# Kernel tuning notes

Hardware: AMD Instinct MI355X
Metric: run time of the kernel (lower is better)

The kernel has to match this reference:

```python
import jax, jax.numpy as jnp
import numpy as np

N_HOST, N_FLOW, E = 20000, 200000, 600000
D_IN, D_H, D_OUT = 64, 128, 32
NEG_SLOPE = 0.01  # F.leaky_relu default


def setup_inputs() -> dict:
    key = jax.random.key(0)
    ks = jax.random.split(key, 20)

    def w(k, shape):
        # kaiming-uniform-ish init scale (matches Linear fan-in scaling)
        lim = 1.0 / np.sqrt(shape[0])
        return jax.random.uniform(k, shape, jnp.float32, -lim, lim)

    return {
        "x_host": jax.random.normal(ks[0], (N_HOST, D_IN), jnp.float32),
        "x_flow": jax.random.normal(ks[1], (N_FLOW, D_IN), jnp.float32),
        "src_hf": jax.random.randint(ks[2], (E,), 0, N_HOST, dtype=jnp.int32),
        "dst_hf": jax.random.randint(ks[3], (E,), 0, N_FLOW, dtype=jnp.int32),
        "src_fh": jax.random.randint(ks[4], (E,), 0, N_FLOW, dtype=jnp.int32),
        "dst_fh": jax.random.randint(ks[5], (E,), 0, N_HOST, dtype=jnp.int32),
        "W0_hf_l": w(ks[6], (D_IN, D_H)), "W0_hf_r": w(ks[7], (D_IN, D_H)),
        "b0_hf": jnp.zeros((D_H,), jnp.float32),
        "W0_fh_l": w(ks[8], (D_IN, D_H)), "W0_fh_r": w(ks[9], (D_IN, D_H)),
        "b0_fh": jnp.zeros((D_H,), jnp.float32),
        "W1_hf_l": w(ks[10], (D_H, D_H)), "W1_hf_r": w(ks[11], (D_H, D_H)),
        "b1_hf": jnp.zeros((D_H,), jnp.float32),
        "W1_fh_l": w(ks[12], (D_H, D_H)), "W1_fh_r": w(ks[13], (D_H, D_H)),
        "b1_fh": jnp.zeros((D_H,), jnp.float32),
        "W_out": w(ks[14], (D_H, D_OUT)),
        "b_out": jnp.zeros((D_OUT,), jnp.float32),
    }


def _seg_mean(x, src, dst, n_dst):
    """Mean-aggregate src-node features over edges into n_dst segments."""
    s = jax.ops.segment_sum(x[src], dst, num_segments=n_dst)      # [n_dst, d]
    cnt = jax.ops.segment_sum(jnp.ones(src.shape, x.dtype), dst, num_segments=n_dst)
    return s / jnp.clip(cnt, 1.0)[:, None]


def _sage(x_src, x_dst, src, dst, Wl, Wr, b, n_dst):
    # SAGEConv: lin_l(mean_agg) + bias + lin_r(x_dst)
    agg = _seg_mean(x_src, src, dst, n_dst)
    return agg @ Wl + b + x_dst @ Wr


def reference(x_host, x_flow, src_hf, dst_hf, src_fh, dst_fh,
              W0_hf_l, W0_hf_r, b0_hf, W0_fh_l, W0_fh_r, b0_fh,
              W1_hf_l, W1_hf_r, b1_hf, W1_fh_l, W1_fh_r, b1_fh,
              W_out, b_out):
    lrelu = lambda v: jnp.where(v > 0, v, NEG_SLOPE * v)

    # layer 0
    h_flow = lrelu(_sage(x_host, x_flow, src_hf, dst_hf, W0_hf_l, W0_hf_r, b0_hf, N_FLOW))
    h_host = lrelu(_sage(x_flow, x_host, src_fh, dst_fh, W0_fh_l, W0_fh_r, b0_fh, N_HOST))

    # layer 1
    g_flow = lrelu(_sage(h_host, h_flow, src_hf, dst_hf, W1_hf_l, W1_hf_r, b1_hf, N_FLOW))
    g_host = lrelu(_sage(h_flow, h_host, src_fh, dst_fh, W1_fh_l, W1_fh_r, b1_fh, N_HOST))
    del g_host  # computed (matches module) but only 'flow' feeds the head

    return g_flow @ W_out + b_out  # [N_FLOW, D_OUT]
```

## Files before the change

kernel.cpp:

```cpp
#include <hip/hip_runtime.h>


#define N_HOST 20000
#define N_FLOW 200000
#define NEDGE  600000
#define D_IN   64
#define D_H    128
#define D_OUT  32
#define NSEG   (N_FLOW + N_HOST)
#define NBKT_F 782
#define NBKT_H 313
#define NBKT   (NBKT_F + NBKT_H)
#define NBKT_PAD 1100
#define NEB    586

typedef unsigned short u16;
typedef unsigned int   u32;
typedef short bf16x8 __attribute__((ext_vector_type(8)));
typedef float f32x4  __attribute__((ext_vector_type(4)));
typedef float fx2    __attribute__((ext_vector_type(2)));
typedef unsigned int u32x4 __attribute__((ext_vector_type(4)));

__device__ __forceinline__ float bfh(u16 h) { return __uint_as_float(((u32)h) << 16); }
__device__ __forceinline__ u16 fbh(float f) {
    u32 u = __float_as_uint(f);
    return (u16)((u + 0x7fffu + ((u >> 16) & 1u)) >> 16);
}
__device__ __forceinline__ u32 packbf(float x, float y) {
    return (u32)fbh(x) | ((u32)fbh(y) << 16);
}
__device__ __forceinline__ void accp(fx2* a, uint4 u) {
    fx2 p;
    p.x = __uint_as_float(u.x << 16); p.y = __uint_as_float(u.x & 0xffff0000u); a[0] += p;
    p.x = __uint_as_float(u.y << 16); p.y = __uint_as_float(u.y & 0xffff0000u); a[1] += p;
    p.x = __uint_as_float(u.z << 16); p.y = __uint_as_float(u.z & 0xffff0000u); a[2] += p;
    p.x = __uint_as_float(u.w << 16); p.y = __uint_as_float(u.w & 0xffff0000u); a[3] += p;
}
__device__ __forceinline__ uint4 packp(const fx2* a, float inv) {
    uint4 o;
    o.x = packbf(a[0].x * inv, a[0].y * inv);
    o.y = packbf(a[1].x * inv, a[1].y * inv);
    o.z = packbf(a[2].x * inv, a[2].y * inv);
    o.w = packbf(a[3].x * inv, a[3].y * inv);
    return o;
}

template <int U>
__device__ __forceinline__ uint4 gmean(const u16* __restrict__ pool, int rs, int coff,
                                       const int* __restrict__ gcsr,
                                       const int* __restrict__ lcsr, int st0, bool fit,
                                       int st, int en) {
    fx2 a[4] = {};
    for (int e = st; e < en; e += U) {
        int n[U];
#pragma unroll
        for (int j = 0; j < U; j++)
            n[j] = (e + j < en) ? (fit ? lcsr[e + j - st0] : gcsr[e + j]) : -1;
        uint4 u[U];
#pragma unroll
        for (int j = 0; j < U; j++)
            u[j] = (n[j] >= 0) ? *(const uint4*)(pool + n[j] * rs + coff)
                               : make_uint4(0u, 0u, 0u, 0u);
#pragma unroll
        for (int j = 0; j < U; j++) accp(a, u[j]);
    }
    float inv = (en > st) ? 1.f / (float)(en - st) : 0.f;
    return packp(a, inv);
}

__global__ void k_pre(const float* __restrict__ W0_hf_l, const float* __restrict__ W0_hf_r,
                      const float* __restrict__ W0_fh_l, const float* __restrict__ W0_fh_r,
                      const float* __restrict__ W1_l, const float* __restrict__ W1_r,
                      const float* __restrict__ Wout,
                      u16* __restrict__ WT0_hf, u16* __restrict__ WT0_fh,
                      u16* __restrict__ WT1_l, u16* __restrict__ WT1_r,
                      u16* __restrict__ WTo,
                      const float* __restrict__ xf, const float* __restrict__ xh,
                      u16* __restrict__ xfb, u16* __restrict__ xhb,
                      const int* __restrict__ dst_hf, const int* __restrict__ dst_fh,
                      int* __restrict__ bcnt) {
    int b = blockIdx.x, t = threadIdx.x;
    if (b < 34) {
        u16 tmp[8];
        if (b < 32) {
            int e = (b & 7) * 2048 + t * 8;
            int n = e >> 7, k0 = e & 127;
            if (b < 8) {
#pragma unroll
                for (int j = 0; j < 8; j++) {
                    int k = k0 + j;
                    tmp[j] = fbh(k < 64 ? W0_hf_l[k * D_H + n] : W0_hf_r[(k - 64) * D_H + n]);
                }
                *(uint4*)(WT0_hf + n * 128 + k0) = *(uint4*)tmp;
            } else if (b < 16) {
#pragma unroll
                for (int j = 0; j < 8; j++) {
                    int k = k0 + j;
                    tmp[j] = fbh(k < 64 ? W0_fh_l[k * D_H + n] : W0_fh_r[(k - 64) * D_H + n]);
                }
                *(uint4*)(WT0_fh + n * 128 + k0) = *(uint4*)tmp;
            } else if (b < 24) {
#pragma unroll
                for (int j = 0; j < 8; j++) tmp[j] = fbh(W1_l[(k0 + j) * D_H + n]);
                *(uint4*)(WT1_l + n * 128 + k0) = *(uint4*)tmp;
            } else {
#pragma unroll
                for (int j = 0; j < 8; j++) tmp[j] = fbh(W1_r[(k0 + j) * D_H + n]);
                *(uint4*)(WT1_r + n * 128 + k0) = *(uint4*)tmp;
            }
        } else {
            int e = (b - 32) * 2048 + t * 8;
            int n = e >> 7, k0 = e & 127;
#pragma unroll
            for (int j = 0; j < 8; j++) tmp[j] = fbh(Wout[(k0 + j) * D_OUT + n]);
            *(uint4*)(WTo + n * 128 + k0) = *(uint4*)tmp;
        }
    } else if (b < 34 + 6875) {
        int q = (b - 34) * 256 + t;
        const int TF = (N_FLOW * D_IN) / 8;
        const int TT = TF + (N_HOST * D_IN) / 8;
        if (q >= TT) return;
        const float* src; u16* dst; int base;
        if (q < TF) { src = xf; dst = xfb; base = q * 8; }
        else        { src = xh; dst = xhb; base = (q - TF) * 8; }
        float4 f0 = *(const float4*)(src + base);
        float4 f1 = *(const float4*)(src + base + 4);
        uint4 o;
        o.x = packbf(f0.x, f0.y); o.y = packbf(f0.z, f0.w);
        o.z = packbf(f1.x, f1.y); o.w = packbf(f1.z, f1.w);
        *(uint4*)(dst + base) = o;
    } else {
        __shared__ int h[NBKT];
        for (int j = t; j < NBKT; j += 256) h[j] = 0;
        __syncthreads();
        int base = (b - 34 - 6875) * 2048;
#pragma unroll
        for (int i = 0; i < 8; i++) {
            int e = base + t + i * 256;
            if (e < 2 * NEDGE) {
                int bkt = (e < NEDGE) ? (dst_hf[e] >> 8)
                                      : (NBKT_F + (dst_fh[e - NEDGE] >> 6));
                atomicAdd(&h[bkt], 1);
            }
        }
        __syncthreads();
        for (int j = t; j < NBKT; j += 256)
            if (h[j]) atomicAdd(&bcnt[j], h[j]);
    }
}

__global__ __launch_bounds__(256) void kb2(
    const int* __restrict__ src_hf, const int* __restrict__ dst_hf,
    const int* __restrict__ src_fh, const int* __restrict__ dst_fh,
    const int* __restrict__ bcnt, int* __restrict__ bcur,
    int2* __restrict__ binE) {
    __shared__ int spx[NBKT_PAD];
    __shared__ int ts[256];
    __shared__ int lh[NBKT];
    __shared__ int lb[NBKT];
    int t = threadIdx.x;
    int v[5], loc[5];
    int b5 = t * 5, s = 0;
#pragma unroll
    for (int j = 0; j < 5; j++) {
        int idx = b5 + j;
        v[j] = (idx < NBKT) ? bcnt[idx] : 0;
        loc[j] = s; s += v[j];
    }
    ts[t] = s;
    for (int j = t; j < NBKT; j += 256) lh[j] = 0;
    __syncthreads();
    for (int d = 1; d < 256; d <<= 1) {
        int x = (t >= d) ? ts[t - d] : 0;
        __syncthreads();
        ts[t] += x;
        __syncthreads();
    }
    int ex = ts[t] - s;
#pragma unroll
    for (int j = 0; j < 5; j++) {
        int idx = b5 + j;
        if (idx < NBKT_PAD) spx[idx] = ex + loc[j];
    }
    __syncthreads();
    int base = blockIdx.x * 2048;
    int mybkt[8], myrank[8], mysrc[8], mydst[8];
#pragma unroll
    for (int i = 0; i < 8; i++) {
        int e = base + t + i * 256;
        mybkt[i] = -1;
        if (e < 2 * NEDGE) {
            int sv, d;
            if (e < NEDGE) { sv = src_hf[e]; d = dst_hf[e]; }
            else           { sv = src_fh[e - NEDGE]; d = dst_fh[e - NEDGE] + N_FLOW; }
            int bkt = (d < N_FLOW) ? (d >> 8) : (NBKT_F + ((d - N_FLOW) >> 6));
            mybkt[i] = bkt; mysrc[i] = sv; mydst[i] = d;
            myrank[i] = atomicAdd(&lh[bkt], 1);
        }
    }
    __syncthreads();
    for (int j = t; j < NBKT; j += 256)
        lb[j] = lh[j] ? atomicAdd(&bcur[j], lh[j]) : 0;
    __syncthreads();
#pragma unroll
    for (int i = 0; i < 8; i++) {
        if (mybkt[i] >= 0) {
            int pos = spx[mybkt[i]] + lb[mybkt[i]] + myrank[i];
            binE[pos] = make_int2(mysrc[i], mydst[i]);
        }
    }
}

__global__ __launch_bounds__(256) void kb3(const int2* __restrict__ binE,
                                           const int* __restrict__ bcnt,
                                           int* __restrict__ off, int* __restrict__ csr) {
    __shared__ int sinc[NBKT_PAD];
    __shared__ int ts[256];
    __shared__ int deg[256];
    int b = blockIdx.x, t = threadIdx.x;
    int v[5], iv[5];
    int b5 = t * 5, s = 0;
#pragma unroll
    for (int j = 0; j < 5; j++) {
        int idx = b5 + j;
        v[j] = (idx < NBKT) ? bcnt[idx] : 0;
        s += v[j]; iv[j] = s;
    }
    ts[t] = s;
    __syncthreads();
    for (int d = 1; d < 256; d <<= 1) {
        int x = (t >= d) ? ts[t - d] : 0;
        __syncthreads();
        ts[t] += x;
        __syncthreads();
    }
    int ex = ts[t] - s;
#pragma unroll
    for (int j = 0; j < 5; j++) {
        int idx = b5 + j;
        if (idx < NBKT_PAD) sinc[idx] = ex + iv[j];
    }
    deg[t] = 0;
    __syncthreads();
    int e0 = (b == 0) ? 0 : sinc[b - 1];
    int e1 = sinc[b];
    int nbase, ncnt;
    if (b < NBKT_F) { nbase = b << 8; ncnt = min(256, N_FLOW - nbase); }
    else { int hb = b - NBKT_F; nbase = N_FLOW + (hb << 6); ncnt = min(64, NSEG - nbase); }
    for (int e = e0 + t; e < e1; e += 256) {
        int2 p = binE[e];
        atomicAdd(&deg[p.y - nbase], 1);
    }
    __syncthreads();
    int myd = deg[t];
    ts[t] = myd;
    __syncthreads();
    for (int d = 1; d < 256; d <<= 1) {
        int x = (t >= d) ? ts[t - d] : 0;
        __syncthreads();
        ts[t] += x;
        __syncthreads();
    }
    int st_ = e0 + ts[t] - myd;
    __syncthreads();
    deg[t] = st_;
    if (t < ncnt) off[nbase + t] = st_ + myd;
    __syncthreads();
    for (int e = e0 + t; e < e1; e += 256) {
        int2 p = binE[e];
        int r = atomicAdd(&deg[p.y - nbase], 1);
        csr[r] = p.x;
    }
}

__global__ __launch_bounds__(512, 4) void k_host(
    const u16* __restrict__ xfb, const u16* __restrict__ xhb,
    const int* __restrict__ off, const int* __restrict__ csr,
    const u16* __restrict__ WT0, const float* __restrict__ b0,
    const u16* __restrict__ WT1l, u16* __restrict__ hT, int M) {
    __shared__ __align__(16) u16 sA[64 * 136];
    __shared__ int sOff[72];
    __shared__ int sCsr[2560];
    const int t = threadIdx.x;
    const int m0 = blockIdx.x * 64;
    if (t < 65) {
        int idx = N_FLOW + m0 - 1 + t;
        sOff[t] = off[min(idx, NSEG - 1)];
    }
    {
        int r = t >> 3, c = t & 7;
        int row = m0 + r;
        uint4 v = make_uint4(0u, 0u, 0u, 0u);
        if (row < M) v = *(const uint4*)(xhb + row * 64 + c * 8);
        *(uint4*)(&sA[r * 136 + 64 + c * 8]) = v;
    }
    __syncthreads();
    int st0 = sOff[0];
    int win = sOff[64] - st0;
    bool fit = (win <= 2560);
    if (fit) for (int e = t; e < win; e += 512) sCsr[e] = csr[st0 + e];
    __syncthreads();
    {
        int r = t >> 3, c = t & 7;
        int row = m0 + r;
        uint4 o = make_uint4(0u, 0u, 0u, 0u);
        if (row < M) o = gmean<8>(xfb, 64, c * 8, csr, sCsr, st0, fit, sOff[r], sOff[r + 1]);
        *(uint4*)(&sA[r * 136 + c * 8]) = o;
    }
    __syncthreads();
    const int w = t >> 6, wr = w >> 1, wc = w & 1;
    const int ln = t & 63, l15 = ln & 15, quad = ln >> 4;
    const u16* pA = sA + (wr * 16 + l15) * 136 + quad * 8;
    const u16* pB0 = WT0 + wc * 8192 + l15 * 128 + quad * 8;
    f32x4 acc[4];
#pragma unroll
    for (int tt = 0; tt < 4; tt++) acc[tt] = (f32x4){0.f, 0.f, 0.f, 0.f};
#pragma unroll
    for (int s = 0; s < 4; s++) {
        bf16x8 a = *(const bf16x8*)(pA + s * 32);
#pragma unroll
        for (int tt = 0; tt < 4; tt++) {
            bf16x8 b = *(const bf16x8*)(pB0 + tt * 2048 + s * 32);
            acc[tt] = __builtin_amdgcn_mfma_f32_16x16x32_bf16(a, b, acc[tt], 0, 0, 0);
        }
    }
    __syncthreads();
#pragma unroll
    for (int tt = 0; tt < 4; tt++) {
        int col = wc * 64 + tt * 16 + l15;
        float bv = b0[col];
#pragma unroll
        for (int i = 0; i < 4; i++) {
            int rl = wr * 16 + quad * 4 + i;
            float v = acc[tt][i] + bv;
            v = v > 0.f ? v : 0.01f * v;
            sA[rl * 136 + col] = fbh(v);
        }
    }
    __syncthreads();
    const u16* pB1 = WT1l + wc * 8192 + l15 * 128 + quad * 8;
    f32x4 accB[4];
#pragma unroll
    for (int tt = 0; tt < 4; tt++) accB[tt] = (f32x4){0.f, 0.f, 0.f, 0.f};
#pragma unroll
    for (int s = 0; s < 4; s++) {
        bf16x8 a = *(const bf16x8*)(pA + s * 32);
#pragma unroll
        for (int tt = 0; tt < 4; tt++) {
            bf16x8 b = *(const bf16x8*)(pB1 + tt * 2048 + s * 32);
            accB[tt] = __builtin_amdgcn_mfma_f32_16x16x32_bf16(a, b, accB[tt], 0, 0, 0);
        }
    }
#pragma unroll
    for (int tt = 0; tt < 4; tt++) {
        int col = wc * 64 + tt * 16 + l15;
#pragma unroll
        for (int i = 0; i < 4; i++) {
            int row = m0 + wr * 16 + quad * 4 + i;
            if (row < M) hT[row * D_H + col] = fbh(accB[tt][i]);
        }
    }
}

__global__ __launch_bounds__(512, 8) void k_mega(
    const u16* __restrict__ xfb, const u16* __restrict__ xhb,
    const int* __restrict__ off, const int* __restrict__ csr,
    const u16* __restrict__ hT,
    const u16* __restrict__ WT0, const float* __restrict__ b0,
    const u16* __restrict__ WT1r, const float* __restrict__ b1,
    const u16* __restrict__ WTo, const float* __restrict__ bout,
    float* __restrict__ OUT) {
    __shared__ __align__(16) u16 sA[64 * 136];
    __shared__ __align__(16) u16 sAg[64 * 136];
    __shared__ int sOff[72];
    __shared__ int sCsr[1024];
    const int t = threadIdx.x;
    const int m0 = blockIdx.x * 64;
    if (t < 65) {
        int idx = m0 - 1 + t;
        sOff[t] = (idx < 0) ? 0 : off[idx];
    }
    {
        int r = t >> 3, c = t & 7;
        const u32x4* p = (const u32x4*)(xfb + (m0 + r) * 64 + c * 8);
        u32x4 v = __builtin_nontemporal_load(p);
        *(u32x4*)(&sA[r * 136 + 64 + c * 8]) = v;
    }
    __syncthreads();
    int st0 = sOff[0];
    int win = sOff[64] - st0;
    bool fit = (win <= 1024);
    if (fit) for (int e = t; e < win; e += 512)
        sCsr[e] = __builtin_nontemporal_load(csr + st0 + e);
    __syncthreads();
    {
        int r = t >> 3, c = t & 7;
        uint4 o = gmean<4>(xhb, 64, c * 8, csr, sCsr, st0, fit, sOff[r], sOff[r + 1]);
        *(uint4*)(&sA[r * 136 + c * 8]) = o;
    }
#pragma unroll
    for (int i = 0; i < 2; i++) {
        int q = t + i * 512;
        int r = q >> 4, c = q & 15;
        uint4 o = gmean<4>(hT, 128, c * 8, csr, sCsr, st0, fit, sOff[r], sOff[r + 1]);
        *(uint4*)(&sAg[r * 136 + c * 8]) = o;
    }
    __syncthreads();
    const int w = t >> 6, wr = w >> 1, wc = w & 1;
    const int ln = t & 63, l15 = ln & 15, quad = ln >> 4;
    const u16* pA = sA + (wr * 16 + l15) * 136 + quad * 8;
    const u16* pB0 = WT0 + wc * 8192 + l15 * 128 + quad * 8;
    f32x4 acc[4];
#pragma unroll
    for (int tt = 0; tt < 4; tt++) acc[tt] = (f32x4){0.f, 0.f, 0.f, 0.f};
#pragma unroll
    for (int s = 0; s < 4; s++) {
        bf16x8 av = *(const bf16x8*)(pA + s * 32);
#pragma unroll
        for (int tt = 0; tt < 4; tt++) {
            bf16x8 b = *(const bf16x8*)(pB0 + tt * 2048 + s * 32);
            acc[tt] = __builtin_amdgcn_mfma_f32_16x16x32_bf16(av, b, acc[tt], 0, 0, 0);
        }
    }
    __syncthreads();
#pragma unroll
    for (int tt = 0; tt < 4; tt++) {
        int col = wc * 64 + tt * 16 + l15;
        float bv = b0[col];
#pragma unroll
        for (int i = 0; i < 4; i++) {
            int rl = wr * 16 + quad * 4 + i;
            float v = acc[tt][i] + bv;
            v = v > 0.f ? v : 0.01f * v;
            sA[rl * 136 + col] = fbh(v);
        }
    }
    __syncthreads();
    const u16* pB1 = WT1r + wc * 8192 + l15 * 128 + quad * 8;
    f32x4 accB[4];
#pragma unroll
    for (int tt = 0; tt < 4; tt++) accB[tt] = (f32x4){0.f, 0.f, 0.f, 0.f};
#pragma unroll
    for (int s = 0; s < 4; s++) {
        bf16x8 av = *(const bf16x8*)(pA + s * 32);
#pragma unroll
        for (int tt = 0; tt < 4; tt++) {
            bf16x8 b = *(const bf16x8*)(pB1 + tt * 2048 + s * 32);
            accB[tt] = __builtin_amdgcn_mfma_f32_16x16x32_bf16(av, b, accB[tt], 0, 0, 0);
        }
    }
#pragma unroll
    for (int tt = 0; tt < 4; tt++) {
        int col = wc * 64 + tt * 16 + l15;
        float bv = b1[col];
#pragma unroll
        for (int i = 0; i < 4; i++) {
            int rl = wr * 16 + quad * 4 + i;
            float v = accB[tt][i] + bfh(sAg[rl * 136 + col]) + bv;
            v = v > 0.f ? v : 0.01f * v;
            sAg[rl * 136 + col] = fbh(v);
        }
    }
    __syncthreads();
    const u16* pG = sAg + (wr * 16 + l15) * 136 + quad * 8;
    const u16* pBo = WTo + wc * 2048 + l15 * 128 + quad * 8;
    f32x4 acc2 = (f32x4){0.f, 0.f, 0.f, 0.f};
#pragma unroll
    for (int s = 0; s < 4; s++) {
        bf16x8 g = *(const bf16x8*)(pG + s * 32);
        bf16x8 b = *(const bf16x8*)(pBo + s * 32);
        acc2 = __builtin_amdgcn_mfma_f32_16x16x32_bf16(g, b, acc2, 0, 0, 0);
    }
    {
        int col = wc * 16 + l15;
        float bv = bout[col];
#pragma unroll
        for (int i = 0; i < 4; i++) {
            int row = m0 + wr * 16 + quad * 4 + i;
            __builtin_nontemporal_store(acc2[i] + bv, &OUT[row * D_OUT + col]);
        }
    }
}

extern "C" void kernel_launch(void* const* d_in, const int* in_sizes, int n_in,
                              void* d_out, int out_size, void* d_ws, size_t ws_size,
                              hipStream_t stream) {
    const float* x_host  = (const float*)d_in[0];
    const float* x_flow  = (const float*)d_in[1];
    const int* src_hf  = (const int*)d_in[2];
    const int* dst_hf  = (const int*)d_in[3];
    const int* src_fh  = (const int*)d_in[4];
    const int* dst_fh  = (const int*)d_in[5];
    const float* W0_hf_l = (const float*)d_in[6];
    const float* W0_hf_r = (const float*)d_in[7];
    const float* b0_hf   = (const float*)d_in[8];
    const float* W0_fh_l = (const float*)d_in[9];
    const float* W0_fh_r = (const float*)d_in[10];
    const float* b0_fh   = (const float*)d_in[11];
    const float* W1_hf_l = (const float*)d_in[12];
    const float* W1_hf_r = (const float*)d_in[13];
    const float* b1_hf   = (const float*)d_in[14];
    const float* W_out   = (const float*)d_in[18];
    const float* b_out   = (const float*)d_in[19];
    float* out = (float*)d_out;

    char* ws = (char*)d_ws;
    int*  off    = (int*)(ws + 0);
    int*  csr    = (int*)(ws + 880000);
    u16*  hT     = (u16*)(ws + 5680000);
    int*  bcnt   = (int*)(ws + 5680000);
    int*  bcur   = (int*)(ws + 5684380);
    u16*  xfb    = (u16*)(ws + 10800000);
    u16*  xhb    = (u16*)(ws + 36400000);
    int2* binE   = (int2*)(ws + 38960000);
    u16*  WT0_hf = (u16*)(ws + 48562560);
    u16*  WT0_fh = (u16*)(ws + 48595328);
    u16*  WT1_l  = (u16*)(ws + 48628096);
    u16*  WT1_r  = (u16*)(ws + 48660864);
    u16*  WTo    = (u16*)(ws + 48693632);

    (void)hipMemsetAsync(bcnt, 0, 8760, stream);
    k_pre<<<34 + 6875 + NEB, 256, 0, stream>>>(
        W0_hf_l, W0_hf_r, W0_fh_l, W0_fh_r, W1_hf_l, W1_hf_r, W_out,
        WT0_hf, WT0_fh, WT1_l, WT1_r, WTo,
        x_flow, x_host, xfb, xhb, dst_hf, dst_fh, bcnt);
    kb2<<<NEB, 256, 0, stream>>>(src_hf, dst_hf, src_fh, dst_fh, bcnt, bcur, binE);
    kb3<<<NBKT, 256, 0, stream>>>(binE, bcnt, off, csr);
    k_host<<<313, 512, 0, stream>>>(xfb, xhb, off, csr, WT0_fh, b0_fh, WT1_l, hT, N_HOST);
    k_mega<<<3125, 512, 0, stream>>>(xfb, xhb, off, csr, hT, WT0_hf, b0_hf,
                                     WT1_r, b1_hf, WTo, b_out, out);
}
```

Measured before the change: 337.5 us.

## Merge graph CSR build stages into one cooperative kernel with grid syncs

```diff
diff --git a/kernel.cpp b/kernel.cpp
--- a/kernel.cpp
+++ b/kernel.cpp
@@ -1,4 +1,6 @@
 #include <hip/hip_runtime.h>
+#include <hip/hip_cooperative_groups.h>
+namespace cg = cooperative_groups;
 
 
 #define N_HOST 20000
@@ -76,9 +78,7 @@
                       u16* __restrict__ WT1_l, u16* __restrict__ WT1_r,
                       u16* __restrict__ WTo,
                       const float* __restrict__ xf, const float* __restrict__ xh,
-                      u16* __restrict__ xfb, u16* __restrict__ xhb,
-                      const int* __restrict__ dst_hf, const int* __restrict__ dst_fh,
-                      int* __restrict__ bcnt) {
+                      u16* __restrict__ xfb, u16* __restrict__ xhb) {
     int b = blockIdx.x, t = threadIdx.x;
     if (b < 34) {
         u16 tmp[8];
@@ -115,7 +115,7 @@
             for (int j = 0; j < 8; j++) tmp[j] = fbh(Wout[(k0 + j) * D_OUT + n]);
             *(uint4*)(WTo + n * 128 + k0) = *(uint4*)tmp;
         }
-    } else if (b < 34 + 6875) {
+    } else {
         int q = (b - 34) * 256 + t;
         const int TF = (N_FLOW * D_IN) / 8;
         const int TT = TF + (N_HOST * D_IN) / 8;
@@ -129,147 +129,158 @@
         o.x = packbf(f0.x, f0.y); o.y = packbf(f0.z, f0.w);
         o.z = packbf(f1.x, f1.y); o.w = packbf(f1.z, f1.w);
         *(uint4*)(dst + base) = o;
-    } else {
-        __shared__ int h[NBKT];
-        for (int j = t; j < NBKT; j += 256) h[j] = 0;
-        __syncthreads();
-        int base = (b - 34 - 6875) * 2048;
+    }
+}
+
+__global__ __launch_bounds__(256) void k_graph(
+    const int* __restrict__ src_hf, const int* __restrict__ dst_hf,
+    const int* __restrict__ src_fh, const int* __restrict__ dst_fh,
+    int* __restrict__ bcnt, int* __restrict__ bcur,
+    int2* __restrict__ binE, int* __restrict__ off, int* __restrict__ csr) {
+    __shared__ int sh_h[NBKT];
+    __shared__ int sh_spx[NBKT_PAD];
+    __shared__ int sh_lb[NBKT];
+    __shared__ int sh_ts[256];
+    __shared__ int sh_deg[256];
+    cg::grid_group grid = cg::this_grid();
+    const int b = blockIdx.x, t = threadIdx.x;
+
+    {
+        int i = b * 256 + t;
+        if (i < NBKT) { bcnt[i] = 0; bcur[i] = 0; }
+    }
+    __threadfence();
+    grid.sync();
+
+    if (b < NEB) {
+        for (int j = t; j < NBKT; j += 256) sh_h[j] = 0;
+        __syncthreads();
+        int base = b * 2048;
 #pragma unroll
         for (int i = 0; i < 8; i++) {
             int e = base + t + i * 256;
             if (e < 2 * NEDGE) {
                 int bkt = (e < NEDGE) ? (dst_hf[e] >> 8)
                                       : (NBKT_F + (dst_fh[e - NEDGE] >> 6));
-                atomicAdd(&h[bkt], 1);
+                atomicAdd(&sh_h[bkt], 1);
             }
         }
         __syncthreads();
         for (int j = t; j < NBKT; j += 256)
-            if (h[j]) atomicAdd(&bcnt[j], h[j]);
-    }
-}
-
-__global__ __launch_bounds__(256) void kb2(
-    const int* __restrict__ src_hf, const int* __restrict__ dst_hf,
-    const int* __restrict__ src_fh, const int* __restrict__ dst_fh,
-    const int* __restrict__ bcnt, int* __restrict__ bcur,
-    int2* __restrict__ binE) {
-    __shared__ int spx[NBKT_PAD];
-    __shared__ int ts[256];
-    __shared__ int lh[NBKT];
-    __shared__ int lb[NBKT];
-    int t = threadIdx.x;
-    int v[5], loc[5];
-    int b5 = t * 5, s = 0;
-#pragma unroll
-    for (int j = 0; j < 5; j++) {
-        int idx = b5 + j;
-        v[j] = (idx < NBKT) ? bcnt[idx] : 0;
-        loc[j] = s; s += v[j];
-    }
-    ts[t] = s;
-    for (int j = t; j < NBKT; j += 256) lh[j] = 0;
-    __syncthreads();
-    for (int d = 1; d < 256; d <<= 1) {
-        int x = (t >= d) ? ts[t - d] : 0;
-        __syncthreads();
-        ts[t] += x;
-        __syncthreads();
-    }
-    int ex = ts[t] - s;
-#pragma unroll
-    for (int j = 0; j < 5; j++) {
-        int idx = b5 + j;
-        if (idx < NBKT_PAD) spx[idx] = ex + loc[j];
-    }
-    __syncthreads();
-    int base = blockIdx.x * 2048;
-    int mybkt[8], myrank[8], mysrc[8], mydst[8];
-#pragma unroll
-    for (int i = 0; i < 8; i++) {
-        int e = base + t + i * 256;
-        mybkt[i] = -1;
-        if (e < 2 * NEDGE) {
-            int sv, d;
-            if (e < NEDGE) { sv = src_hf[e]; d = dst_hf[e]; }
-            else           { sv = src_fh[e - NEDGE]; d = dst_fh[e - NEDGE] + N_FLOW; }
-            int bkt = (d < N_FLOW) ? (d >> 8) : (NBKT_F + ((d - N_FLOW) >> 6));
-            mybkt[i] = bkt; mysrc[i] = sv; mydst[i] = d;
-            myrank[i] = atomicAdd(&lh[bkt], 1);
-        }
-    }
-    __syncthreads();
-    for (int j = t; j < NBKT; j += 256)
-        lb[j] = lh[j] ? atomicAdd(&bcur[j], lh[j]) : 0;
-    __syncthreads();
-#pragma unroll
-    for (int i = 0; i < 8; i++) {
-        if (mybkt[i] >= 0) {
-            int pos = spx[mybkt[i]] + lb[mybkt[i]] + myrank[i];
-            binE[pos] = make_int2(mysrc[i], mydst[i]);
-        }
-    }
-}
-
-__global__ __launch_bounds__(256) void kb3(const int2* __restrict__ binE,
-                                           const int* __restrict__ bcnt,
-                                           int* __restrict__ off, int* __restrict__ csr) {
-    __shared__ int sinc[NBKT_PAD];
-    __shared__ int ts[256];
-    __shared__ int deg[256];
-    int b = blockIdx.x, t = threadIdx.x;
-    int v[5], iv[5];
-    int b5 = t * 5, s = 0;
-#pragma unroll
-    for (int j = 0; j < 5; j++) {
-        int idx = b5 + j;
-        v[j] = (idx < NBKT) ? bcnt[idx] : 0;
-        s += v[j]; iv[j] = s;
-    }
-    ts[t] = s;
-    __syncthreads();
-    for (int d = 1; d < 256; d <<= 1) {
-        int x = (t >= d) ? ts[t - d] : 0;
-        __syncthreads();
-        ts[t] += x;
-        __syncthreads();
-    }
-    int ex = ts[t] - s;
-#pragma unroll
-    for (int j = 0; j < 5; j++) {
-        int idx = b5 + j;
-        if (idx < NBKT_PAD) sinc[idx] = ex + iv[j];
-    }
-    deg[t] = 0;
-    __syncthreads();
-    int e0 = (b == 0) ? 0 : sinc[b - 1];
-    int e1 = sinc[b];
-    int nbase, ncnt;
-    if (b < NBKT_F) { nbase = b << 8; ncnt = min(256, N_FLOW - nbase); }
-    else { int hb = b - NBKT_F; nbase = N_FLOW + (hb << 6); ncnt = min(64, NSEG - nbase); }
-    for (int e = e0 + t; e < e1; e += 256) {
-        int2 p = binE[e];
-        atomicAdd(&deg[p.y - nbase], 1);
-    }
-    __syncthreads();
-    int myd = deg[t];
-    ts[t] = myd;
-    __syncthreads();
-    for (int d = 1; d < 256; d <<= 1) {
-        int x = (t >= d) ? ts[t - d] : 0;
-        __syncthreads();
-        ts[t] += x;
-        __syncthreads();
-    }
-    int st_ = e0 + ts[t] - myd;
-    __syncthreads();
-    deg[t] = st_;
-    if (t < ncnt) off[nbase + t] = st_ + myd;
-    __syncthreads();
-    for (int e = e0 + t; e < e1; e += 256) {
-        int2 p = binE[e];
-        int r = atomicAdd(&deg[p.y - nbase], 1);
-        csr[r] = p.x;
+            if (sh_h[j]) atomicAdd(&bcnt[j], sh_h[j]);
+    }
+    __threadfence();
+    grid.sync();
+
+    if (b < NEB) {
+        int v[5], loc[5];
+        int b5 = t * 5, s = 0;
+#pragma unroll
+        for (int j = 0; j < 5; j++) {
+            int idx = b5 + j;
+            v[j] = (idx < NBKT) ? bcnt[idx] : 0;
+            loc[j] = s; s += v[j];
+        }
+        sh_ts[t] = s;
+        for (int j = t; j < NBKT; j += 256) sh_h[j] = 0;
+        __syncthreads();
+        for (int d = 1; d < 256; d <<= 1) {
+            int x = (t >= d) ? sh_ts[t - d] : 0;
+            __syncthreads();
+            sh_ts[t] += x;
+            __syncthreads();
+        }
+        int ex = sh_ts[t] - s;
+#pragma unroll
+        for (int j = 0; j < 5; j++) {
+            int idx = b5 + j;
+            if (idx < NBKT_PAD) sh_spx[idx] = ex + loc[j];
+        }
+        __syncthreads();
+        int base = b * 2048;
+        int mybkt[8], myrank[8], mysrc[8], mydst[8];
+#pragma unroll
+        for (int i = 0; i < 8; i++) {
+            int e = base + t + i * 256;
+            mybkt[i] = -1;
+            if (e < 2 * NEDGE) {
+                int sv, d;
+                if (e < NEDGE) { sv = src_hf[e]; d = dst_hf[e]; }
+                else           { sv = src_fh[e - NEDGE]; d = dst_fh[e - NEDGE] + N_FLOW; }
+                int bkt = (d < N_FLOW) ? (d >> 8) : (NBKT_F + ((d - N_FLOW) >> 6));
+                mybkt[i] = bkt; mysrc[i] = sv; mydst[i] = d;
+                myrank[i] = atomicAdd(&sh_h[bkt], 1);
+            }
+        }
+        __syncthreads();
+        for (int j = t; j < NBKT; j += 256)
+            sh_lb[j] = sh_h[j] ? atomicAdd(&bcur[j], sh_h[j]) : 0;
+        __syncthreads();
+#pragma unroll
+        for (int i = 0; i < 8; i++) {
+            if (mybkt[i] >= 0) {
+                int pos = sh_spx[mybkt[i]] + sh_lb[mybkt[i]] + myrank[i];
+                binE[pos] = make_int2(mysrc[i], mydst[i]);
+            }
+        }
+    }
+    __threadfence();
+    grid.sync();
+
+    {
+        int v[5], iv[5];
+        int b5 = t * 5, s = 0;
+#pragma unroll
+        for (int j = 0; j < 5; j++) {
+            int idx = b5 + j;
+            v[j] = (idx < NBKT) ? bcnt[idx] : 0;
+            s += v[j]; iv[j] = s;
+        }
+        sh_ts[t] = s;
+        __syncthreads();
+        for (int d = 1; d < 256; d <<= 1) {
+            int x = (t >= d) ? sh_ts[t - d] : 0;
+            __syncthreads();
+            sh_ts[t] += x;
+            __syncthreads();
+        }
+        int ex = sh_ts[t] - s;
+#pragma unroll
+        for (int j = 0; j < 5; j++) {
+            int idx = b5 + j;
+            if (idx < NBKT_PAD) sh_spx[idx] = ex + iv[j];
+        }
+        sh_deg[t] = 0;
+        __syncthreads();
+        int e0 = (b == 0) ? 0 : sh_spx[b - 1];
+        int e1 = sh_spx[b];
+        int nbase, ncnt;
+        if (b < NBKT_F) { nbase = b << 8; ncnt = min(256, N_FLOW - nbase); }
+        else { int hb = b - NBKT_F; nbase = N_FLOW + (hb << 6); ncnt = min(64, NSEG - nbase); }
+        for (int e = e0 + t; e < e1; e += 256) {
+            int2 p = binE[e];
+            atomicAdd(&sh_deg[p.y - nbase], 1);
+        }
+        __syncthreads();
+        int myd = sh_deg[t];
+        sh_ts[t] = myd;
+        __syncthreads();
+        for (int d = 1; d < 256; d <<= 1) {
+            int x = (t >= d) ? sh_ts[t - d] : 0;
+            __syncthreads();
+            sh_ts[t] += x;
+            __syncthreads();
+        }
+        int st_ = e0 + sh_ts[t] - myd;
+        __syncthreads();
+        sh_deg[t] = st_;
+        if (t < ncnt) off[nbase + t] = st_ + myd;
+        __syncthreads();
+        for (int e = e0 + t; e < e1; e += 256) {
+            int2 p = binE[e];
+            int r = atomicAdd(&sh_deg[p.y - nbase], 1);
+            csr[r] = p.x;
+        }
     }
 }
 
@@ -519,13 +530,17 @@
     u16*  WT1_r  = (u16*)(ws + 48660864);
     u16*  WTo    = (u16*)(ws + 48693632);
 
-    (void)hipMemsetAsync(bcnt, 0, 8760, stream);
-    k_pre<<<34 + 6875 + NEB, 256, 0, stream>>>(
+    k_pre<<<34 + 6875, 256, 0, stream>>>(
         W0_hf_l, W0_hf_r, W0_fh_l, W0_fh_r, W1_hf_l, W1_hf_r, W_out,
         WT0_hf, WT0_fh, WT1_l, WT1_r, WTo,
-        x_flow, x_host, xfb, xhb, dst_hf, dst_fh, bcnt);
-    kb2<<<NEB, 256, 0, stream>>>(src_hf, dst_hf, src_fh, dst_fh, bcnt, bcur, binE);
-    kb3<<<NBKT, 256, 0, stream>>>(binE, bcnt, off, csr);
+        x_flow, x_host, xfb, xhb);
+    {
+        void* kargs[] = {(void*)&src_hf, (void*)&dst_hf, (void*)&src_fh, (void*)&dst_fh,
+                         (void*)&bcnt, (void*)&bcur, (void*)&binE, (void*)&off,
+                         (void*)&csr};
+        (void)hipLaunchCooperativeKernel((const void*)k_graph, dim3(NBKT), dim3(256),
+                                         kargs, 0, stream);
+    }
     k_host<<<313, 512, 0, stream>>>(xfb, xhb, off, csr, WT0_fh, b0_fh, WT1_l, hT, N_HOST);
     k_mega<<<3125, 512, 0, stream>>>(xfb, xhb, off, csr, hT, WT0_hf, b0_hf,
                                      WT1_r, b1_hf, WTo, b_out, out);
```

New measurement: 897.4 us. 166% more time.
